# Optimization experiments

Hardware: AMD Instinct MI355X
Metric: run time of the kernel (lower is better)

The kernel has to match this reference:

```python
import jax, jax.numpy as jnp
import numpy as np

LEAKY_SLOPE = 0.01  # PyTorch F.leaky_relu default


def setup_inputs() -> dict:
    key = jax.random.key(0)
    ks = jax.random.split(key, 6)
    N, E, IN, OUT = 100000, 1000000, 256, 64
    x = jax.random.normal(ks[0], (N, IN), dtype=jnp.float32)
    edge_index = jax.random.randint(ks[1], (2, E), 0, N, dtype=jnp.int64)
    edge_weight = jax.random.uniform(ks[2], (E,), dtype=jnp.float32)
    W_lin = jax.random.normal(ks[3], (IN, OUT), dtype=jnp.float32) / np.sqrt(IN)
    b_lin = jax.random.normal(ks[4], (OUT,), dtype=jnp.float32) * 0.01
    W_att = jax.random.normal(ks[5], (2 * OUT, 1), dtype=jnp.float32) / np.sqrt(2 * OUT)
    b_att = jnp.zeros((1,), dtype=jnp.float32)
    return {"x": x, "edge_index": edge_index, "edge_weight": edge_weight,
            "W_lin": W_lin, "b_lin": b_lin, "W_att": W_att, "b_att": b_att}


def reference(x, edge_index, edge_weight, W_lin, b_lin, W_att, b_att):
    # h = Linear(x): [N, OUT]
    h = x @ W_lin + b_lin
    row, col = edge_index[0], edge_index[1]
    OUT = h.shape[-1]
    # attention(cat([h_i, h_j])) == h_i @ W_att[:OUT] + h_j @ W_att[OUT:] + b_att.
    # Project per-node first (N x OUT GEMV) then gather scalars per edge — same math,
    # avoids materializing the [E, 2*OUT] concatenation.
    a_src = (h @ W_att[:OUT]).squeeze(-1)   # [N]
    a_dst = (h @ W_att[OUT:]).squeeze(-1)   # [N]
    scores = a_src[row] + a_dst[col] + b_att[0]          # [E]
    scores = jax.nn.leaky_relu(scores, LEAKY_SLOPE)
    # Global softmax over all edges (dim=0 in the original on an [E,1] tensor)
    scores = jax.nn.softmax(scores, axis=0)
    scores = scores * edge_weight                        # [E]
    msgs = scores[:, None] * h[col]                      # [E, OUT]
    agg = jnp.zeros_like(h).at[row].add(msgs)            # scatter-add to [N, OUT]
    return jax.nn.relu(h + agg)
```

## Files before the change

kernel.cpp:

```cpp
#include <hip/hip_runtime.h>

#define LEAKY 0.01f
#define CAP 15

typedef __attribute__((ext_vector_type(8))) short short8;
typedef __attribute__((ext_vector_type(4))) float f32x4;

__device__ __forceinline__ unsigned short f2bf(float f) {
    unsigned u = __float_as_uint(f);
    return (unsigned short)((u + 0x7FFFu + ((u >> 16) & 1u)) >> 16);
}
__device__ __forceinline__ float bf2f(unsigned short u) {
    return __uint_as_float((unsigned)u << 16);
}

__global__ __launch_bounds__(256) void k_prep(
    const float* __restrict__ W, unsigned short* __restrict__ wt,
    float* __restrict__ gsum)
{
    int t = blockIdx.x * 256 + threadIdx.x;
    if (t == 0) *gsum = 0.f;
    int n = t >> 8;
    int k = t & 255;
    unsigned short bf = f2bf(W[k * 64 + n]);
    int slot = (k >> 3) ^ (n & 7);
    wt[(n * 512 + slot * 16 + (k & 7) * 2) >> 1] = bf;
}

__global__ __launch_bounds__(256, 4) void k_linear(
    const float* __restrict__ x, const unsigned short* __restrict__ wt_g,
    const float* __restrict__ bl, const float* __restrict__ Wa,
    unsigned short* __restrict__ hb, float* __restrict__ a_dst,
    unsigned* __restrict__ ell, int N)
{
    __shared__ __align__(16) char wtlds[32768];
    int t = threadIdx.x;
    int r0 = blockIdx.x * 64;

    #pragma unroll
    for (int i = 0; i < 8; ++i) {
        int f8 = t + i * 256;
        ((uint4*)wtlds)[f8] = ((const uint4*)wt_g)[f8];
    }
    __syncthreads();

    int lane = t & 63;
    int w = t >> 6;
    int cl = lane & 15;
    int lg = lane >> 4;

    int arow = w * 16 + cl;
    int grow = r0 + arow;
    const float* xrow = x + (size_t)min(grow, N - 1) * 256;

    short8 a[8];
    #pragma unroll
    for (int kk = 0; kk < 8; ++kk) {
        int k0 = (kk * 4 + lg) * 8;
        float4 v0 = *(const float4*)(xrow + k0);
        float4 v1 = *(const float4*)(xrow + k0 + 4);
        short8 av;
        av[0] = (short)f2bf(v0.x); av[1] = (short)f2bf(v0.y);
        av[2] = (short)f2bf(v0.z); av[3] = (short)f2bf(v0.w);
        av[4] = (short)f2bf(v1.x); av[5] = (short)f2bf(v1.y);
        av[6] = (short)f2bf(v1.z); av[7] = (short)f2bf(v1.w);
        a[kk] = av;
    }

    f32x4 acc[4];
    #pragma unroll
    for (int n = 0; n < 4; ++n) acc[n] = (f32x4){0.f, 0.f, 0.f, 0.f};

    #pragma unroll
    for (int n = 0; n < 4; ++n) {
        int brow = n * 16 + cl;
        #pragma unroll
        for (int kk = 0; kk < 8; ++kk) {
            int ak = kk * 4 + lg;
            short8 bfr = *(const short8*)(wtlds + brow * 512 + ((ak ^ (brow & 7)) << 4));
            acc[n] = __builtin_amdgcn_mfma_f32_16x16x32_bf16(a[kk], bfr, acc[n], 0, 0, 0);
        }
    }

    float asj[4] = {0.f, 0.f, 0.f, 0.f}, adj[4] = {0.f, 0.f, 0.f, 0.f};
    #pragma unroll
    for (int n = 0; n < 4; ++n) {
        int col = n * 16 + cl;
        float bias = bl[col];
        float wa1 = Wa[col], wa2 = Wa[64 + col];
        #pragma unroll
        for (int j = 0; j < 4; ++j) {
            float hv = acc[n][j] + bias;
            int gr = r0 + w * 16 + lg * 4 + j;
            if (gr < N) hb[(size_t)gr * 64 + col] = f2bf(hv);
            asj[j] = fmaf(hv, wa1, asj[j]);
            adj[j] = fmaf(hv, wa2, adj[j]);
        }
    }
    #pragma unroll
    for (int off = 1; off < 16; off <<= 1) {
        #pragma unroll
        for (int j = 0; j < 4; ++j) {
            asj[j] += __shfl_xor(asj[j], off);
            adj[j] += __shfl_xor(adj[j], off);
        }
    }
    if (cl == 0) {
        #pragma unroll
        for (int j = 0; j < 4; ++j) {
            int gr = r0 + w * 16 + lg * 4 + j;
            if (gr < N) {
                a_dst[gr] = adj[j];
                ell[(size_t)gr * 16] = (unsigned)f2bf(asj[j]) << 16;
            }
        }
    }
}

__global__ __launch_bounds__(256) void k_bucket(
    const int* __restrict__ ei, const float* __restrict__ ew,
    const float* __restrict__ a_dst, const float* __restrict__ batt,
    unsigned* __restrict__ ell, float* __restrict__ gsum, int E)
{
    int e0 = (blockIdx.x * 256 + threadIdx.x) * 4;
    float psum = 0.f;
    if (e0 + 3 < E) {
        int4 rr = *(const int4*)(ei + e0);
        int4 cc = *(const int4*)(ei + E + e0);
        float4 wv = *(const float4*)(ew + e0);
        float b = batt[0];
        unsigned* r0 = ell + (size_t)rr.x * 16;
        unsigned* r1 = ell + (size_t)rr.y * 16;
        unsigned* r2 = ell + (size_t)rr.z * 16;
        unsigned* r3 = ell + (size_t)rr.w * 16;
        unsigned o0 = atomicAdd(r0, 1u);
        unsigned o1 = atomicAdd(r1, 1u);
        unsigned o2 = atomicAdd(r2, 1u);
        unsigned o3 = atomicAdd(r3, 1u);
        float s0 = bf2f((unsigned short)(o0 >> 16)) + a_dst[cc.x] + b;
        float s1 = bf2f((unsigned short)(o1 >> 16)) + a_dst[cc.y] + b;
        float s2 = bf2f((unsigned short)(o2 >> 16)) + a_dst[cc.z] + b;
        float s3 = bf2f((unsigned short)(o3 >> 16)) + a_dst[cc.w] + b;
        s0 = (s0 > 0.f) ? s0 : LEAKY * s0;
        s1 = (s1 > 0.f) ? s1 : LEAKY * s1;
        s2 = (s2 > 0.f) ? s2 : LEAKY * s2;
        s3 = (s3 > 0.f) ? s3 : LEAKY * s3;
        float p0 = __expf(s0), p1 = __expf(s1), p2 = __expf(s2), p3 = __expf(s3);
        unsigned k0 = o0 & 0xFFFFu, k1 = o1 & 0xFFFFu;
        unsigned k2 = o2 & 0xFFFFu, k3 = o3 & 0xFFFFu;
        if (k0 < CAP) r0[1 + k0] = ((unsigned)cc.x << 15) | ((__float_as_uint(p0 * wv.x) >> 16) & 0x7FFFu);
        if (k1 < CAP) r1[1 + k1] = ((unsigned)cc.y << 15) | ((__float_as_uint(p1 * wv.y) >> 16) & 0x7FFFu);
        if (k2 < CAP) r2[1 + k2] = ((unsigned)cc.z << 15) | ((__float_as_uint(p2 * wv.z) >> 16) & 0x7FFFu);
        if (k3 < CAP) r3[1 + k3] = ((unsigned)cc.w << 15) | ((__float_as_uint(p3 * wv.w) >> 16) & 0x7FFFu);
        psum = (p0 + p1) + (p2 + p3);
    } else {
        for (int e = e0; e < E; ++e) {
            int r = ei[e], c = ei[E + e];
            unsigned* rw = ell + (size_t)r * 16;
            unsigned o = atomicAdd(rw, 1u);
            float s = bf2f((unsigned short)(o >> 16)) + a_dst[c] + batt[0];
            s = (s > 0.f) ? s : LEAKY * s;
            float p = __expf(s);
            unsigned k = o & 0xFFFFu;
            if (k < CAP) rw[1 + k] =
                ((unsigned)c << 15) | ((__float_as_uint(p * ew[e]) >> 16) & 0x7FFFu);
            psum += p;
        }
    }
    #pragma unroll
    for (int off = 32; off; off >>= 1) psum += __shfl_xor(psum, off);
    __shared__ float wsum[4];
    int lane = threadIdx.x & 63, w = threadIdx.x >> 6;
    if (lane == 0) wsum[w] = psum;
    __syncthreads();
    if (threadIdx.x == 0) atomicAdd(gsum, wsum[0] + wsum[1] + wsum[2] + wsum[3]);
}

__global__ __launch_bounds__(256) void k_aggregate(
    const unsigned* __restrict__ ell, const unsigned short* __restrict__ hb,
    const float* __restrict__ gsum, float4* __restrict__ out4, int N)
{
    int r = blockIdx.x * 4 + (threadIdx.x >> 6);
    if (r >= N) return;
    int lane = threadIdx.x & 63;
    int sub = lane >> 4, l = lane & 15;
    const unsigned* row = ell + (size_t)r * 16;
    int d = min((int)(row[0] & 0xFFFFu), CAP);
    float4 acc = make_float4(0.f, 0.f, 0.f, 0.f);
    for (int p = sub; p < d; p += 4) {
        unsigned rec = row[1 + p];
        float cf = __uint_as_float((rec & 0x7FFFu) << 16);
        int c = rec >> 15;
        ushort4 hv = *(const ushort4*)(hb + (size_t)c * 64 + l * 4);
        acc.x = fmaf(cf, bf2f(hv.x), acc.x);
        acc.y = fmaf(cf, bf2f(hv.y), acc.y);
        acc.z = fmaf(cf, bf2f(hv.z), acc.z);
        acc.w = fmaf(cf, bf2f(hv.w), acc.w);
    }
    acc.x += __shfl_xor(acc.x, 16); acc.y += __shfl_xor(acc.y, 16);
    acc.z += __shfl_xor(acc.z, 16); acc.w += __shfl_xor(acc.w, 16);
    acc.x += __shfl_xor(acc.x, 32); acc.y += __shfl_xor(acc.y, 32);
    acc.z += __shfl_xor(acc.z, 32); acc.w += __shfl_xor(acc.w, 32);
    if (sub == 0) {
        float inv = 1.0f / (*gsum);
        ushort4 hv = *(const ushort4*)(hb + (size_t)r * 64 + l * 4);
        float4 o;
        o.x = fmaxf(fmaf(inv, acc.x, bf2f(hv.x)), 0.f);
        o.y = fmaxf(fmaf(inv, acc.y, bf2f(hv.y)), 0.f);
        o.z = fmaxf(fmaf(inv, acc.z, bf2f(hv.z)), 0.f);
        o.w = fmaxf(fmaf(inv, acc.w, bf2f(hv.w)), 0.f);
        out4[(size_t)r * 16 + l] = o;
    }
}

extern "C" void kernel_launch(void* const* d_in, const int* in_sizes, int n_in,
                              void* d_out, int out_size, void* d_ws, size_t ws_size,
                              hipStream_t stream)
{
    const float* x    = (const float*)d_in[0];
    const int*   ei   = (const int*)d_in[1];
    const float* ew   = (const float*)d_in[2];
    const float* Wlin = (const float*)d_in[3];
    const float* blin = (const float*)d_in[4];
    const float* Watt = (const float*)d_in[5];
    const float* batt = (const float*)d_in[6];
    float* out = (float*)d_out;

    int N = in_sizes[0] / 256;
    int E = in_sizes[2];

    char* p = (char*)d_ws;
    unsigned short* hb = (unsigned short*)p; p += (size_t)N * 64 * 2;
    float* a_dst    = (float*)p;  p += (size_t)N * 4;
    unsigned short* wt = (unsigned short*)p; p += 65536;
    float* gsum     = (float*)p;  p += 64;
    unsigned* ell   = (unsigned*)p;

    k_prep<<<64, 256, 0, stream>>>(Wlin, wt, gsum);
    k_linear<<<(N + 63) / 64, 256, 0, stream>>>(x, wt, blin, Watt, hb,
                                                a_dst, ell, N);
    k_bucket<<<(E / 4 + 255) / 256, 256, 0, stream>>>(ei, ew, a_dst, batt,
                                                      ell, gsum, E);
    k_aggregate<<<(N + 3) / 4, 256, 0, stream>>>(ell, hb, gsum, (float4*)out, N);
}
```

Before: 131.7 us.

## Partition edge bucketing by destination row across XCD-aligned block groups

Each group of 8 consecutive blocks reads the same 2048-edge chunk. Each block handles only the edges whose row index mod 8 equals its blockIdx mod 8, so atomics and ELL writes for a given row stay on one XCD's L2. The source attention term is now stored as a separate fp32 array instead of being packed as bf16 into the ELL header and returned by the atomic. The cost is that the edge index and weight arrays are read 8 times, and there is an extra gather per edge.

```diff
diff --git a/kernel.cpp b/kernel.cpp
--- a/kernel.cpp
+++ b/kernel.cpp
@@ -30,8 +30,8 @@
 __global__ __launch_bounds__(256, 4) void k_linear(
     const float* __restrict__ x, const unsigned short* __restrict__ wt_g,
     const float* __restrict__ bl, const float* __restrict__ Wa,
-    unsigned short* __restrict__ hb, float* __restrict__ a_dst,
-    unsigned* __restrict__ ell, int N)
+    unsigned short* __restrict__ hb, float* __restrict__ a_src,
+    float* __restrict__ a_dst, unsigned* __restrict__ ell, int N)
 {
     __shared__ __align__(16) char wtlds[32768];
     int t = threadIdx.x;
@@ -110,8 +110,9 @@
         for (int j = 0; j < 4; ++j) {
             int gr = r0 + w * 16 + lg * 4 + j;
             if (gr < N) {
+                a_src[gr] = asj[j];
                 a_dst[gr] = adj[j];
-                ell[(size_t)gr * 16] = (unsigned)f2bf(asj[j]) << 16;
+                ell[(size_t)gr * 16] = 0u;
             }
         }
     }
@@ -119,52 +120,53 @@
 
 __global__ __launch_bounds__(256) void k_bucket(
     const int* __restrict__ ei, const float* __restrict__ ew,
-    const float* __restrict__ a_dst, const float* __restrict__ batt,
-    unsigned* __restrict__ ell, float* __restrict__ gsum, int E)
-{
-    int e0 = (blockIdx.x * 256 + threadIdx.x) * 4;
+    const float* __restrict__ a_src, const float* __restrict__ a_dst,
+    const float* __restrict__ batt, unsigned* __restrict__ ell,
+    float* __restrict__ gsum, int E)
+{
+    int part = blockIdx.x & 7;
+    int chunk = blockIdx.x >> 3;
+    int base = chunk * 2048;
+    float b = batt[0];
     float psum = 0.f;
-    if (e0 + 3 < E) {
-        int4 rr = *(const int4*)(ei + e0);
-        int4 cc = *(const int4*)(ei + E + e0);
-        float4 wv = *(const float4*)(ew + e0);
-        float b = batt[0];
-        unsigned* r0 = ell + (size_t)rr.x * 16;
-        unsigned* r1 = ell + (size_t)rr.y * 16;
-        unsigned* r2 = ell + (size_t)rr.z * 16;
-        unsigned* r3 = ell + (size_t)rr.w * 16;
-        unsigned o0 = atomicAdd(r0, 1u);
-        unsigned o1 = atomicAdd(r1, 1u);
-        unsigned o2 = atomicAdd(r2, 1u);
-        unsigned o3 = atomicAdd(r3, 1u);
-        float s0 = bf2f((unsigned short)(o0 >> 16)) + a_dst[cc.x] + b;
-        float s1 = bf2f((unsigned short)(o1 >> 16)) + a_dst[cc.y] + b;
-        float s2 = bf2f((unsigned short)(o2 >> 16)) + a_dst[cc.z] + b;
-        float s3 = bf2f((unsigned short)(o3 >> 16)) + a_dst[cc.w] + b;
-        s0 = (s0 > 0.f) ? s0 : LEAKY * s0;
-        s1 = (s1 > 0.f) ? s1 : LEAKY * s1;
-        s2 = (s2 > 0.f) ? s2 : LEAKY * s2;
-        s3 = (s3 > 0.f) ? s3 : LEAKY * s3;
-        float p0 = __expf(s0), p1 = __expf(s1), p2 = __expf(s2), p3 = __expf(s3);
-        unsigned k0 = o0 & 0xFFFFu, k1 = o1 & 0xFFFFu;
-        unsigned k2 = o2 & 0xFFFFu, k3 = o3 & 0xFFFFu;
-        if (k0 < CAP) r0[1 + k0] = ((unsigned)cc.x << 15) | ((__float_as_uint(p0 * wv.x) >> 16) & 0x7FFFu);
-        if (k1 < CAP) r1[1 + k1] = ((unsigned)cc.y << 15) | ((__float_as_uint(p1 * wv.y) >> 16) & 0x7FFFu);
-        if (k2 < CAP) r2[1 + k2] = ((unsigned)cc.z << 15) | ((__float_as_uint(p2 * wv.z) >> 16) & 0x7FFFu);
-        if (k3 < CAP) r3[1 + k3] = ((unsigned)cc.w << 15) | ((__float_as_uint(p3 * wv.w) >> 16) & 0x7FFFu);
-        psum = (p0 + p1) + (p2 + p3);
-    } else {
-        for (int e = e0; e < E; ++e) {
-            int r = ei[e], c = ei[E + e];
-            unsigned* rw = ell + (size_t)r * 16;
-            unsigned o = atomicAdd(rw, 1u);
-            float s = bf2f((unsigned short)(o >> 16)) + a_dst[c] + batt[0];
-            s = (s > 0.f) ? s : LEAKY * s;
-            float p = __expf(s);
-            unsigned k = o & 0xFFFFu;
-            if (k < CAP) rw[1 + k] =
-                ((unsigned)c << 15) | ((__float_as_uint(p * ew[e]) >> 16) & 0x7FFFu);
-            psum += p;
+
+    #pragma unroll
+    for (int it = 0; it < 2; ++it) {
+        int e0 = base + it * 1024 + threadIdx.x * 4;
+        if (e0 + 3 < E) {
+            int4 rr = *(const int4*)(ei + e0);
+            int4 cc = *(const int4*)(ei + E + e0);
+            float4 wv = *(const float4*)(ew + e0);
+            int r[4] = {rr.x, rr.y, rr.z, rr.w};
+            int c[4] = {cc.x, cc.y, cc.z, cc.w};
+            float wvv[4] = {wv.x, wv.y, wv.z, wv.w};
+            #pragma unroll
+            for (int q = 0; q < 4; ++q) {
+                if ((r[q] & 7) == part) {
+                    float s = a_src[r[q]] + a_dst[c[q]] + b;
+                    s = (s > 0.f) ? s : LEAKY * s;
+                    float p = __expf(s);
+                    unsigned* rw = ell + (size_t)r[q] * 16;
+                    unsigned k = atomicAdd(rw, 1u);
+                    if (k < CAP) rw[1 + k] = ((unsigned)c[q] << 15) |
+                        ((__float_as_uint(p * wvv[q]) >> 16) & 0x7FFFu);
+                    psum += p;
+                }
+            }
+        } else {
+            for (int e = e0; e < E && e < e0 + 4; ++e) {
+                int r = ei[e], c = ei[E + e];
+                if ((r & 7) == part) {
+                    float s = a_src[r] + a_dst[c] + b;
+                    s = (s > 0.f) ? s : LEAKY * s;
+                    float p = __expf(s);
+                    unsigned* rw = ell + (size_t)r * 16;
+                    unsigned k = atomicAdd(rw, 1u);
+                    if (k < CAP) rw[1 + k] = ((unsigned)c << 15) |
+                        ((__float_as_uint(p * ew[e]) >> 16) & 0x7FFFu);
+                    psum += p;
+                }
+            }
         }
     }
     #pragma unroll
@@ -231,6 +233,7 @@
 
     char* p = (char*)d_ws;
     unsigned short* hb = (unsigned short*)p; p += (size_t)N * 64 * 2;
+    float* a_src    = (float*)p;  p += (size_t)N * 4;
     float* a_dst    = (float*)p;  p += (size_t)N * 4;
     unsigned short* wt = (unsigned short*)p; p += 65536;
     float* gsum     = (float*)p;  p += 64;
@@ -238,8 +241,9 @@
 
     k_prep<<<64, 256, 0, stream>>>(Wlin, wt, gsum);
     k_linear<<<(N + 63) / 64, 256, 0, stream>>>(x, wt, blin, Watt, hb,
-                                                a_dst, ell, N);
-    k_bucket<<<(E / 4 + 255) / 256, 256, 0, stream>>>(ei, ew, a_dst, batt,
-                                                      ell, gsum, E);
+                                                a_src, a_dst, ell, N);
+    int C = (E + 2047) / 2048;
+    k_bucket<<<C * 8, 256, 0, stream>>>(ei, ew, a_src, a_dst, batt,
+                                        ell, gsum, E);
     k_aggregate<<<(N + 3) / 4, 256, 0, stream>>>(ell, hb, gsum, (float4*)out, N);
 }
```

After: 180.0 us. 1.37x slower.
